# Performance work log

Hardware: AMD Instinct MI355X
Metric: run time of the kernel (lower is better)

The kernel has to match this reference:

```python
import math
import jax, jax.numpy as jnp
import numpy as np

B, S, D = 4, 2048, 1280
H, HD = 16, 80  # num_heads, head_dim
LOG2E = 1.442695041


def setup_inputs() -> dict:
    key = jax.random.key(0)
    ks = jax.random.split(key, 6)
    hidden_states = jax.random.normal(ks[0], (B, S, D), dtype=jnp.float32)
    # additive causal mask: 0 on/below diagonal, large negative above
    causal = jnp.tril(jnp.ones((S, S), dtype=bool))
    attention_mask = jnp.where(causal, 0.0, -1e9).astype(jnp.float32)[None, None, :, :]
    attention_mask = jnp.broadcast_to(attention_mask, (B, 1, S, S))
    scaling = jax.random.normal(ks[1], (HD,), dtype=jnp.float32)
    fan = 1.0 / math.sqrt(D)
    qkv_w = jax.random.normal(ks[2], (3 * H * HD, D), dtype=jnp.float32) * fan
    qkv_b = jax.random.normal(ks[3], (3 * H * HD,), dtype=jnp.float32) * fan
    o_w = jax.random.normal(ks[4], (D, H * HD), dtype=jnp.float32) * (1.0 / math.sqrt(H * HD))
    o_b = jax.random.normal(ks[5], (D,), dtype=jnp.float32) * fan
    return {
        "hidden_states": hidden_states,
        "attention_mask": attention_mask,
        "scaling": scaling,
        "qkv_w": qkv_w,
        "qkv_b": qkv_b,
        "o_w": o_w,
        "o_b": o_b,
    }


def reference(hidden_states, attention_mask, scaling, qkv_w, qkv_b, o_w, o_b):
    b, s, _ = hidden_states.shape
    qkv = hidden_states @ qkv_w.T + qkv_b  # [b, s, 3*H*HD]
    xq, xk, xv = jnp.split(qkv, [H * HD, 2 * H * HD], axis=-1)
    xq = xq.reshape(b, s, H, HD)
    xk = xk.reshape(b, s, H, HD)
    xv = xv.reshape(b, s, H, HD)
    # per-dim query scaling: softplus(scaling) * log2(e) / sqrt(head_dim)
    scale = jax.nn.softplus(scaling) * (LOG2E / math.sqrt(HD))
    xq = xq * scale[None, None, None, :]
    scores = jnp.einsum("bqhd,bkhd->bhqk", xq, xk) + attention_mask  # [b,H,s,s]
    probs = jax.nn.softmax(scores.astype(jnp.float32), axis=-1).astype(xq.dtype)
    out = jnp.einsum("bhqk,bkhd->bqhd", probs, xv).reshape(b, s, H * HD)
    return out @ o_w.T + o_b
```

## Files before the change

### kernel.cpp

```cpp
#include <hip/hip_runtime.h>
#include <math.h>

#define B_ 4
#define S_ 2048
#define D_ 1280
#define H_ 16
#define HD_ 80
#define HHD (H_ * HD_)
#define QKVN (3 * H_ * HD_)

typedef __bf16 bf16x8 __attribute__((ext_vector_type(8)));
typedef __bf16 bf16x4 __attribute__((ext_vector_type(4)));
typedef float  f32x4  __attribute__((ext_vector_type(4)));

__global__ __launch_bounds__(256) void cvt_bf16(
    const float* __restrict__ in, __bf16* __restrict__ out, int n8)
{
    const int i = blockIdx.x * 256 + threadIdx.x;
    if (i < n8) {
        const float4 a = ((const float4*)in)[2 * (size_t)i];
        const float4 b = ((const float4*)in)[2 * (size_t)i + 1];
        bf16x8 v = {(__bf16)a.x, (__bf16)a.y, (__bf16)a.z, (__bf16)a.w,
                    (__bf16)b.x, (__bf16)b.y, (__bf16)b.z, (__bf16)b.w};
        *(bf16x8*)(out + 8 * (size_t)i) = v;
    }
}

__device__ __forceinline__ void async_copy16(const void* g, void* l)
{
    __builtin_amdgcn_global_load_lds(
        (const __attribute__((address_space(1))) unsigned int*)g,
        (__attribute__((address_space(3))) unsigned int*)l, 16, 0, 0);
}

__device__ __forceinline__ void stage128x64(
    const __bf16* __restrict__ src, int K, char* lds, int tid)
{
    const int wave = tid >> 6, lane = tid & 63;
#pragma unroll
    for (int i = 0; i < 4; ++i) {
        const int c = (wave * 4 + i) * 64 + lane;
        const int r = c >> 3;
        const int g = (c & 7) ^ (r & 7);
        async_copy16(src + (size_t)r * K + g * 8, lds + (wave * 4 + i) * 1024);
    }
}

__device__ __forceinline__ bf16x8 frag_ld(const char* lds, int m, int j)
{
    return *(const bf16x8*)(lds + m * 128 + ((j ^ (m & 7)) << 4));
}

__device__ __forceinline__ void mfma_loop(
    const __bf16* __restrict__ A, const __bf16* __restrict__ W, int K,
    char* ldsA, char* ldsB, int tid, f32x4 acc[4][4])
{
    const int wave = tid >> 6;
    const int wm = wave >> 1, wn = wave & 1;
    const int l16 = tid & 15, quad = (tid & 63) >> 4;

#pragma unroll
    for (int mi = 0; mi < 4; ++mi)
#pragma unroll
        for (int ni = 0; ni < 4; ++ni) acc[mi][ni] = (f32x4){0.f, 0.f, 0.f, 0.f};

    for (int k0 = 0; k0 < K; k0 += 64) {
        __syncthreads();
        stage128x64(A + k0, K, ldsA, tid);
        stage128x64(W + k0, K, ldsB, tid);
        __syncthreads();
#pragma unroll
        for (int ks = 0; ks < 2; ++ks) {
            bf16x8 af[4], bfr[4];
#pragma unroll
            for (int mi = 0; mi < 4; ++mi)
                af[mi] = frag_ld(ldsA, wm * 64 + mi * 16 + l16, ks * 4 + quad);
#pragma unroll
            for (int ni = 0; ni < 4; ++ni)
                bfr[ni] = frag_ld(ldsB, wn * 64 + ni * 16 + l16, ks * 4 + quad);
#pragma unroll
            for (int mi = 0; mi < 4; ++mi)
#pragma unroll
                for (int ni = 0; ni < 4; ++ni)
                    acc[mi][ni] = __builtin_amdgcn_mfma_f32_16x16x32_bf16(
                        af[mi], bfr[ni], acc[mi][ni], 0, 0, 0);
        }
    }
}

__device__ __forceinline__ void stage_half256(
    const __bf16* __restrict__ src, int K, char* ldsmat, int half, int tid)
{
    const int wave = tid >> 6, lane = tid & 63;
#pragma unroll
    for (int i = 0; i < 2; ++i) {
        const int c = (i * 8 + wave) * 64 + lane;
        const int r = half * 128 + (c >> 3);
        const int g = (c & 7) ^ (r & 7);
        async_copy16(src + (size_t)r * K + g * 8,
                     ldsmat + half * 16384 + (i * 8 + wave) * 1024);
    }
}

#define QBAR() do { asm volatile("" ::: "memory");                             \
                    __builtin_amdgcn_s_barrier();                              \
                    __builtin_amdgcn_sched_barrier(0); } while (0)

__global__ __launch_bounds__(512, 2) void gemm_qkv_256(
    const __bf16* __restrict__ Ab, const __bf16* __restrict__ Wb,
    const float* __restrict__ bias, const float* __restrict__ scaling,
    __bf16* __restrict__ Qb, __bf16* __restrict__ Kb, __bf16* __restrict__ Vtb)
{
    __shared__ __align__(16) char lds[2][2][32768];
    const int tid = threadIdx.x;
    const int wave = tid >> 6;
    const int wm = wave >> 2, wn = wave & 3;
    const int l16 = tid & 15, quad = (tid & 63) >> 4;

    const int flat = blockIdx.x;
    const int xcd = flat & 7;
    const int idx = flat >> 3;
    const int m_i = idx & 3, n_g = idx >> 2;
    const int m0 = (xcd * 4 + m_i) * 256;
    const int n0 = n_g * 256;

    const __bf16* A = Ab + (size_t)m0 * D_;
    const __bf16* W = Wb + (size_t)n0 * D_;

    f32x4 acc[8][4];
#pragma unroll
    for (int mi = 0; mi < 8; ++mi)
#pragma unroll
        for (int ni = 0; ni < 4; ++ni) acc[mi][ni] = (f32x4){0.f, 0.f, 0.f, 0.f};

    stage_half256(A, D_, lds[0][0], 0, tid);
    stage_half256(A, D_, lds[0][0], 1, tid);
    stage_half256(W, D_, lds[0][1], 0, tid);
    stage_half256(W, D_, lds[0][1], 1, tid);

    const int nt = D_ / 64;
    bf16x8 af[4][2], bfr[2][2];

#define RD_A(MH)                                                               \
    _Pragma("unroll")                                                          \
    for (int mi = 0; mi < 4; ++mi)                                             \
        _Pragma("unroll")                                                      \
        for (int ks = 0; ks < 2; ++ks)                                         \
            af[mi][ks] = frag_ld(lA, wm * 128 + (MH) * 64 + mi * 16 + l16,     \
                                 ks * 4 + quad);
#define RD_B(NH)                                                               \
    _Pragma("unroll")                                                          \
    for (int ni = 0; ni < 2; ++ni)                                             \
        _Pragma("unroll")                                                      \
        for (int ks = 0; ks < 2; ++ks)                                         \
            bfr[ni][ks] = frag_ld(lB, wn * 64 + (NH) * 32 + ni * 16 + l16,     \
                                  ks * 4 + quad);
#define MM16(MH, NH)                                                           \
    __builtin_amdgcn_s_setprio(1);                                             \
    _Pragma("unroll")                                                          \
    for (int mi = 0; mi < 4; ++mi)                                             \
        _Pragma("unroll")                                                      \
        for (int ni = 0; ni < 2; ++ni) {                                       \
            acc[(MH)*4+mi][(NH)*2+ni] = __builtin_amdgcn_mfma_f32_16x16x32_bf16( \
                af[mi][0], bfr[ni][0], acc[(MH)*4+mi][(NH)*2+ni], 0, 0, 0);    \
            acc[(MH)*4+mi][(NH)*2+ni] = __builtin_amdgcn_mfma_f32_16x16x32_bf16( \
                af[mi][1], bfr[ni][1], acc[(MH)*4+mi][(NH)*2+ni], 0, 0, 0);    \
        }                                                                      \
    __builtin_amdgcn_s_setprio(0);

    for (int t = 0; t < nt; ++t) {
        const int cur = t & 1;
        const char* lA = lds[cur][0];
        const char* lB = lds[cur][1];
        char* sA = lds[cur ^ 1][0];
        char* sB = lds[cur ^ 1][1];
        const int kn = (t + 1 < nt ? t + 1 : t) * 64;

        stage_half256(A + kn, D_, sA, 0, tid);
        asm volatile("s_waitcnt vmcnt(2)" ::: "memory");
        QBAR();
        RD_A(0) RD_B(0) MM16(0, 0)
        stage_half256(A + kn, D_, sA, 1, tid);
        RD_B(1) MM16(0, 1)
        stage_half256(W + kn, D_, sB, 0, tid);
        RD_A(1) RD_B(0) MM16(1, 0)
        stage_half256(W + kn, D_, sB, 1, tid);
        RD_B(1) MM16(1, 1)
        QBAR();
    }
#undef RD_A
#undef RD_B
#undef MM16

    const int sec = n_g / 5;
    if (sec == 2) {
#pragma unroll
        for (int ni = 0; ni < 4; ++ni) {
            const int col = n0 + wn * 64 + ni * 16 + l16;
            const int cis = col - 2 * HHD;
            const int h = cis / HD_;
            const int d = cis - h * HD_;
            const float bv = bias[col];
#pragma unroll
            for (int mi = 0; mi < 8; ++mi) {
                const int row0 = m0 + wm * 128 + mi * 16 + quad * 4;
                const int bb = row0 >> 11;
                const int s = row0 & (S_ - 1);
                const size_t bh = (size_t)(bb * H_ + h);
                bf16x4 pv = {(__bf16)(acc[mi][ni][0] + bv),
                             (__bf16)(acc[mi][ni][1] + bv),
                             (__bf16)(acc[mi][ni][2] + bv),
                             (__bf16)(acc[mi][ni][3] + bv)};
                *(bf16x4*)(Vtb + (bh * HD_ + d) * S_ + s) = pv;
            }
        }
    } else {
#pragma unroll
        for (int ni = 0; ni < 4; ++ni) {
            const int col = n0 + wn * 64 + ni * 16 + l16;
            const int cis = col - sec * HHD;
            const int h = cis / HD_;
            const int d = cis - h * HD_;
            const float bv = bias[col];
            float qsv = 0.f;
            if (sec == 0)
                qsv = log1pf(expf(scaling[d])) *
                      (1.442695041f * 1.442695041f / 8.944271910f);
#pragma unroll
            for (int mi = 0; mi < 8; ++mi) {
#pragma unroll
                for (int r = 0; r < 4; ++r) {
                    const int row = m0 + wm * 128 + mi * 16 + quad * 4 + r;
                    const int bb = row >> 11;
                    const int s = row & (S_ - 1);
                    const size_t bh = (size_t)(bb * H_ + h);
                    const float v = acc[mi][ni][r] + bv;
                    if (sec == 0) Qb[(bh * S_ + s) * HD_ + d] = (__bf16)(v * qsv);
                    else          Kb[(bh * S_ + s) * HD_ + d] = (__bf16)v;
                }
            }
        }
    }
}

__global__ __launch_bounds__(256) void gemm_o_mfma(
    const __bf16* __restrict__ Ab, const __bf16* __restrict__ Wb,
    const float* __restrict__ bias, float* __restrict__ C)
{
    __shared__ __align__(16) char ldsA[128 * 128];
    __shared__ __align__(16) char ldsB[128 * 128];
    const int tid = threadIdx.x;

    const int flat = blockIdx.x;
    const int xcd = flat & 7;
    const int idx = flat >> 3;
    const int mm = idx / 10;
    const int nn = idx - mm * 10;
    const int m0 = (xcd * 8 + mm) * 128;
    const int n0 = nn * 128;

    f32x4 acc[4][4];
    mfma_loop(Ab + (size_t)m0 * D_, Wb + (size_t)n0 * D_, D_, ldsA, ldsB, tid, acc);

    const int wave = tid >> 6, wm = wave >> 1, wn = wave & 1;
    const int l16 = tid & 15, quad = (tid & 63) >> 4;

#pragma unroll
    for (int ni = 0; ni < 4; ++ni) {
        const int col = n0 + wn * 64 + ni * 16 + l16;
        const float bv = bias[col];
#pragma unroll
        for (int mi = 0; mi < 4; ++mi) {
#pragma unroll
            for (int r = 0; r < 4; ++r) {
                const int row = m0 + wm * 64 + mi * 16 + quad * 4 + r;
                C[(size_t)row * D_ + col] = acc[mi][ni][r] + bv;
            }
        }
    }
}

struct KF8 { bf16x8 f0, f1, f2; };

__device__ __forceinline__ void kload8(
    const __bf16* __restrict__ base, int row, int quad, KF8& kf)
{
    const __bf16* r = base + (size_t)row * HD_;
    kf.f0 = *(const bf16x8*)(r + quad * 8);
    kf.f1 = *(const bf16x8*)(r + 32 + quad * 8);
    bf16x8 z = {};
    if (quad < 2) z = *(const bf16x8*)(r + 64 + quad * 8);
    kf.f2 = z;
}

#define QK3(SREG, KF, QF)                                                      \
    SREG = __builtin_amdgcn_mfma_f32_16x16x32_bf16(KF.f0, QF.f0, SREG, 0, 0, 0); \
    SREG = __builtin_amdgcn_mfma_f32_16x16x32_bf16(KF.f1, QF.f1, SREG, 0, 0, 0); \
    SREG = __builtin_amdgcn_mfma_f32_16x16x32_bf16(KF.f2, QF.f2, SREG, 0, 0, 0);

#define MASK4(SREG, BASE, Q)                                                   \
    _Pragma("unroll")                                                          \
    for (int i = 0; i < 4; ++i)                                                \
        SREG[i] = ((BASE) + quad * 4 + i <= (Q) + l16) ? SREG[i] : -1e30f;

#define ATTN_BODY64(KT)                                                        \
    {                                                                          \
        const int k0 = (KT) * 64;                                              \
        const bool do_lo = ((KT) < nkt_lo);                  \
        const bf16x8 vf00 = *(const bf16x8*)(Vbase + (size_t)( 0 + l16) * S_ + k0 + quad * 8);      \
        const bf16x8 vf01 = *(const bf16x8*)(Vbase + (size_t)( 0 + l16) * S_ + k0 + 32 + quad * 8); \
        const bf16x8 vf10 = *(const bf16x8*)(Vbase + (size_t)(16 + l16) * S_ + k0 + quad * 8);      \
        const bf16x8 vf11 = *(const bf16x8*)(Vbase + (size_t)(16 + l16) * S_ + k0 + 32 + quad * 8); \
        const bf16x8 vf20 = *(const bf16x8*)(Vbase + (size_t)(32 + l16) * S_ + k0 + quad * 8);      \
        const bf16x8 vf21 = *(const bf16x8*)(Vbase + (size_t)(32 + l16) * S_ + k0 + 32 + quad * 8); \
        const bf16x8 vf30 = *(const bf16x8*)(Vbase + (size_t)(48 + l16) * S_ + k0 + quad * 8);      \
        const bf16x8 vf31 = *(const bf16x8*)(Vbase + (size_t)(48 + l16) * S_ + k0 + 32 + quad * 8); \
        const bf16x8 vf40 = *(const bf16x8*)(Vbase + (size_t)(64 + l16) * S_ + k0 + quad * 8);      \
        const bf16x8 vf41 = *(const bf16x8*)(Vbase + (size_t)(64 + l16) * S_ + k0 + 32 + quad * 8); \
        f32x4 sH0 = (f32x4){0.f,0.f,0.f,0.f}, sH1 = sH0, sH2 = sH0, sH3 = sH0; \
        f32x4 sL0 = sH0, sL1 = sH0, sL2 = sH0, sL3 = sH0;                      \
        __builtin_amdgcn_s_setprio(1);                                         \
        QK3(sH0, kf0, qfH) QK3(sH1, kf1, qfH) QK3(sH2, kf2, qfH) QK3(sH3, kf3, qfH) \
        if (do_lo) {                                                           \
            QK3(sL0, kf0, qfL) QK3(sL1, kf1, qfL)                              \
            QK3(sL2, kf2, qfL) QK3(sL3, kf3, qfL)                              \
        }                                                                      \
        __builtin_amdgcn_s_setprio(0);                                         \
        {                                                                      \
            const int kn = ((KT) + 1 < nkt_hi ? (KT) + 1 : (KT)) * 64;         \
            kload8(Kbase, kn + l16, quad, kf0);                                \
            kload8(Kbase, kn + 16 + l16, quad, kf1);                           \
            kload8(Kbase, kn + 32 + l16, quad, kf2);                           \
            kload8(Kbase, kn + 48 + l16, quad, kf3);                           \
        }                                                                      \
        float aH;                                                              \
        {                                                                      \
            if (k0 + 63 > q_hi) {                                              \
                MASK4(sH0, k0, q_hi)      MASK4(sH1, k0 + 16, q_hi)            \
                MASK4(sH2, k0 + 32, q_hi) MASK4(sH3, k0 + 48, q_hi)            \
            }                                                                  \
            float mA = fmaxf(fmaxf(sH0[0], sH0[1]), fmaxf(sH0[2], sH0[3]));    \
            float mB = fmaxf(fmaxf(sH1[0], sH1[1]), fmaxf(sH1[2], sH1[3]));    \
            float mC = fmaxf(fmaxf(sH2[0], sH2[1]), fmaxf(sH2[2], sH2[3]));    \
            float mD = fmaxf(fmaxf(sH3[0], sH3[1]), fmaxf(sH3[2], sH3[3]));    \
            float mx = fmaxf(fmaxf(mA, mB), fmaxf(mC, mD));                    \
            mx = fmaxf(mx, __shfl_xor(mx, 16));                                \
            mx = fmaxf(mx, __shfl_xor(mx, 32));                                \
            const float mn = fmaxf(mH, mx);                                    \
            aH = exp2f(mH - mn);                                               \
            mH = mn;                                                           \
            float rs = 0.f;                                                    \
            _Pragma("unroll")                                                  \
            for (int i = 0; i < 4; ++i) {                                      \
                const float p0 = exp2f(sH0[i] - mn);                           \
                const float p1 = exp2f(sH1[i] - mn);                           \
                const float p2 = exp2f(sH2[i] - mn);                           \
                const float p3 = exp2f(sH3[i] - mn);                           \
                sH0[i] = p0; sH1[i] = p1; sH2[i] = p2; sH3[i] = p3;            \
                rs += (p0 + p1) + (p2 + p3);                                   \
            }                                                                  \
            lH = lH * aH + rs;                                                 \
            *(bf16x4*)&Ps[wave][0][l16][0][quad * 4] =                         \
                (bf16x4){(__bf16)sH0[0], (__bf16)sH0[1], (__bf16)sH0[2], (__bf16)sH0[3]}; \
            *(bf16x4*)&Ps[wave][0][l16][0][16 + quad * 4] =                    \
                (bf16x4){(__bf16)sH1[0], (__bf16)sH1[1], (__bf16)sH1[2], (__bf16)sH1[3]}; \
            *(bf16x4*)&Ps[wave][0][l16][1][quad * 4] =                         \
                (bf16x4){(__bf16)sH2[0], (__bf16)sH2[1], (__bf16)sH2[2], (__bf16)sH2[3]}; \
            *(bf16x4*)&Ps[wave][0][l16][1][16 + quad * 4] =                    \
                (bf16x4){(__bf16)sH3[0], (__bf16)sH3[1], (__bf16)sH3[2], (__bf16)sH3[3]}; \
        }                                                                      \
        float aL = 1.f;                                                        \
        if (do_lo) {                                                           \
            if (k0 + 63 > q_lo) {                                              \
                MASK4(sL0, k0, q_lo)      MASK4(sL1, k0 + 16, q_lo)            \
                MASK4(sL2, k0 + 32, q_lo) MASK4(sL3, k0 + 48, q_lo)            \
            }                                                                  \
            float mA = fmaxf(fmaxf(sL0[0], sL0[1]), fmaxf(sL0[2], sL0[3]));    \
            float mB = fmaxf(fmaxf(sL1[0], sL1[1]), fmaxf(sL1[2], sL1[3]));    \
            float mC = fmaxf(fmaxf(sL2[0], sL2[1]), fmaxf(sL2[2], sL2[3]));    \
            float mD = fmaxf(fmaxf(sL3[0], sL3[1]), fmaxf(sL3[2], sL3[3]));    \
            float mx = fmaxf(fmaxf(mA, mB), fmaxf(mC, mD));                    \
            mx = fmaxf(mx, __shfl_xor(mx, 16));                                \
            mx = fmaxf(mx, __shfl_xor(mx, 32));                                \
            const float mn = fmaxf(mL, mx);                                    \
            aL = exp2f(mL - mn);                                               \
            mL = mn;                                                           \
            float rs = 0.f;                                                    \
            _Pragma("unroll")                                                  \
            for (int i = 0; i < 4; ++i) {                                      \
                const float p0 = exp2f(sL0[i] - mn);                           \
                const float p1 = exp2f(sL1[i] - mn);                           \
                const float p2 = exp2f(sL2[i] - mn);                           \
                const float p3 = exp2f(sL3[i] - mn);                           \
                sL0[i] = p0; sL1[i] = p1; sL2[i] = p2; sL3[i] = p3;            \
                rs += (p0 + p1) + (p2 + p3);                                   \
            }                                                                  \
            lL = lL * aL + rs;                                                 \
            *(bf16x4*)&Ps[wave][1][l16][0][quad * 4] =                         \
                (bf16x4){(__bf16)sL0[0], (__bf16)sL0[1], (__bf16)sL0[2], (__bf16)sL0[3]}; \
            *(bf16x4*)&Ps[wave][1][l16][0][16 + quad * 4] =                    \
                (bf16x4){(__bf16)sL1[0], (__bf16)sL1[1], (__bf16)sL1[2], (__bf16)sL1[3]}; \
            *(bf16x4*)&Ps[wave][1][l16][1][quad * 4] =                         \
                (bf16x4){(__bf16)sL2[0], (__bf16)sL2[1], (__bf16)sL2[2], (__bf16)sL2[3]}; \
            *(bf16x4*)&Ps[wave][1][l16][1][16 + quad * 4] =                    \
                (bf16x4){(__bf16)sL3[0], (__bf16)sL3[1], (__bf16)sL3[2], (__bf16)sL3[3]}; \
        }                                                                      \
        asm volatile("s_waitcnt lgkmcnt(0)" ::: "memory");                     \
        const bf16x8 pfH0 = *(const bf16x8*)&Ps[wave][0][l16][0][quad * 8];    \
        const bf16x8 pfH1 = *(const bf16x8*)&Ps[wave][0][l16][1][quad * 8];    \
        const bf16x8 pfL0 = *(const bf16x8*)&Ps[wave][1][l16][0][quad * 8];    \
        const bf16x8 pfL1 = *(const bf16x8*)&Ps[wave][1][l16][1][quad * 8];    \
        __builtin_amdgcn_s_setprio(1);                                         \
        {                                                                      \
            f32x4 c0, c1, c2, c3, c4;                                          \
            _Pragma("unroll")                                                  \
            for (int i = 0; i < 4; ++i) {                                      \
                c0[i] = oH0[i] * aH; c1[i] = oH1[i] * aH; c2[i] = oH2[i] * aH; \
                c3[i] = oH3[i] * aH; c4[i] = oH4[i] * aH;                      \
            }                                                                  \
            oH0 = __builtin_amdgcn_mfma_f32_16x16x32_bf16(vf00, pfH0, c0, 0, 0, 0); \
            oH1 = __builtin_amdgcn_mfma_f32_16x16x32_bf16(vf10, pfH0, c1, 0, 0, 0); \
            oH2 = __builtin_amdgcn_mfma_f32_16x16x32_bf16(vf20, pfH0, c2, 0, 0, 0); \
            oH3 = __builtin_amdgcn_mfma_f32_16x16x32_bf16(vf30, pfH0, c3, 0, 0, 0); \
            oH4 = __builtin_amdgcn_mfma_f32_16x16x32_bf16(vf40, pfH0, c4, 0, 0, 0); \
            oH0 = __builtin_amdgcn_mfma_f32_16x16x32_bf16(vf01, pfH1, oH0, 0, 0, 0); \
            oH1 = __builtin_amdgcn_mfma_f32_16x16x32_bf16(vf11, pfH1, oH1, 0, 0, 0); \
            oH2 = __builtin_amdgcn_mfma_f32_16x16x32_bf16(vf21, pfH1, oH2, 0, 0, 0); \
            oH3 = __builtin_amdgcn_mfma_f32_16x16x32_bf16(vf31, pfH1, oH3, 0, 0, 0); \
            oH4 = __builtin_amdgcn_mfma_f32_16x16x32_bf16(vf41, pfH1, oH4, 0, 0, 0); \
        }                                                                      \
        if (do_lo) {                                                           \
            f32x4 c0, c1, c2, c3, c4;                                          \
            _Pragma("unroll")                                                  \
            for (int i = 0; i < 4; ++i) {                                      \
                c0[i] = oL0[i] * aL; c1[i] = oL1[i] * aL; c2[i] = oL2[i] * aL; \
                c3[i] = oL3[i] * aL; c4[i] = oL4[i] * aL;                      \
            }                                                                  \
            oL0 = __builtin_amdgcn_mfma_f32_16x16x32_bf16(vf00, pfL0, c0, 0, 0, 0); \
            oL1 = __builtin_amdgcn_mfma_f32_16x16x32_bf16(vf10, pfL0, c1, 0, 0, 0); \
            oL2 = __builtin_amdgcn_mfma_f32_16x16x32_bf16(vf20, pfL0, c2, 0, 0, 0); \
            oL3 = __builtin_amdgcn_mfma_f32_16x16x32_bf16(vf30, pfL0, c3, 0, 0, 0); \
            oL4 = __builtin_amdgcn_mfma_f32_16x16x32_bf16(vf40, pfL0, c4, 0, 0, 0); \
            oL0 = __builtin_amdgcn_mfma_f32_16x16x32_bf16(vf01, pfL1, oL0, 0, 0, 0); \
            oL1 = __builtin_amdgcn_mfma_f32_16x16x32_bf16(vf11, pfL1, oL1, 0, 0, 0); \
            oL2 = __builtin_amdgcn_mfma_f32_16x16x32_bf16(vf21, pfL1, oL2, 0, 0, 0); \
            oL3 = __builtin_amdgcn_mfma_f32_16x16x32_bf16(vf31, pfL1, oL3, 0, 0, 0); \
            oL4 = __builtin_amdgcn_mfma_f32_16x16x32_bf16(vf41, pfL1, oL4, 0, 0, 0); \
        }                                                                      \
        __builtin_amdgcn_s_setprio(0);                                         \
    }

__global__ __launch_bounds__(256, 2) void attn_v13(
    const __bf16* __restrict__ Qb, const __bf16* __restrict__ Kb,
    const __bf16* __restrict__ Vtb, __bf16* __restrict__ out)
{
    __shared__ __align__(16) __bf16 Ps[4][2][16][2][40];

    const int tid = threadIdx.x;
    const int wave = tid >> 6;
    const int lane = tid & 63;
    const int l16 = lane & 15;
    const int quad = lane >> 4;

    const int flat = blockIdx.x;
    const int c = flat & 7;
    const int slot = flat >> 3;
    const int bhgrp = slot >> 4;
    const int xslot = slot & 15;
    const int bh = bhgrp * 8 + c;
    const int x = (xslot + 5 * bhgrp) & 15;
    const int b = bh >> 4, h = bh & 15;

    const int q_lo = 64 * x + 16 * wave;
    const int q_hi = 64 * (31 - x) + 16 * wave;

    const __bf16* Qbase = Qb + (size_t)bh * S_ * HD_;
    const __bf16* Kbase = Kb + (size_t)bh * S_ * HD_;
    const __bf16* Vbase = Vtb + (size_t)bh * HD_ * S_;

    KF8 qfL, qfH;
    kload8(Qbase, q_lo + l16, quad, qfL);
    kload8(Qbase, q_hi + l16, quad, qfH);

    float mL = -1e30f, lL = 0.f, mH = -1e30f, lH = 0.f;
    f32x4 oH0 = (f32x4){0.f,0.f,0.f,0.f}, oH1 = oH0, oH2 = oH0, oH3 = oH0, oH4 = oH0;
    f32x4 oL0 = oH0, oL1 = oH0, oL2 = oH0, oL3 = oH0, oL4 = oH0;

    const int nkt_lo = (q_lo + 16 + 63) >> 6;
    const int nkt_hi = (q_hi + 16 + 63) >> 6;

    KF8 kf0, kf1, kf2, kf3;
    kload8(Kbase, l16, quad, kf0);
    kload8(Kbase, 16 + l16, quad, kf1);
    kload8(Kbase, 32 + l16, quad, kf2);
    kload8(Kbase, 48 + l16, quad, kf3);

    for (int kt = 0; kt < nkt_hi; ++kt) {
        ATTN_BODY64(kt);
    }

    float lHs = lH + __shfl_xor(lH, 16);
    lHs += __shfl_xor(lHs, 32);
    float lLs = lL + __shfl_xor(lL, 16);
    lLs += __shfl_xor(lLs, 32);
    const float invH = 1.f / lHs;
    const float invL = 1.f / lLs;
    const size_t rowH = ((size_t)b * S_ + q_hi + l16) * HHD + h * HD_ + quad * 4;
    const size_t rowL = ((size_t)b * S_ + q_lo + l16) * HHD + h * HD_ + quad * 4;
    {
        bf16x4 v0 = {(__bf16)(oH0[0]*invH), (__bf16)(oH0[1]*invH), (__bf16)(oH0[2]*invH), (__bf16)(oH0[3]*invH)};
        bf16x4 v1 = {(__bf16)(oH1[0]*invH), (__bf16)(oH1[1]*invH), (__bf16)(oH1[2]*invH), (__bf16)(oH1[3]*invH)};
        bf16x4 v2 = {(__bf16)(oH2[0]*invH), (__bf16)(oH2[1]*invH), (__bf16)(oH2[2]*invH), (__bf16)(oH2[3]*invH)};
        bf16x4 v3 = {(__bf16)(oH3[0]*invH), (__bf16)(oH3[1]*invH), (__bf16)(oH3[2]*invH), (__bf16)(oH3[3]*invH)};
        bf16x4 v4 = {(__bf16)(oH4[0]*invH), (__bf16)(oH4[1]*invH), (__bf16)(oH4[2]*invH), (__bf16)(oH4[3]*invH)};
        *(bf16x4*)(out + rowH)      = v0;
        *(bf16x4*)(out + rowH + 16) = v1;
        *(bf16x4*)(out + rowH + 32) = v2;
        *(bf16x4*)(out + rowH + 48) = v3;
        *(bf16x4*)(out + rowH + 64) = v4;
    }
    {
        bf16x4 v0 = {(__bf16)(oL0[0]*invL), (__bf16)(oL0[1]*invL), (__bf16)(oL0[2]*invL), (__bf16)(oL0[3]*invL)};
        bf16x4 v1 = {(__bf16)(oL1[0]*invL), (__bf16)(oL1[1]*invL), (__bf16)(oL1[2]*invL), (__bf16)(oL1[3]*invL)};
        bf16x4 v2 = {(__bf16)(oL2[0]*invL), (__bf16)(oL2[1]*invL), (__bf16)(oL2[2]*invL), (__bf16)(oL2[3]*invL)};
        bf16x4 v3 = {(__bf16)(oL3[0]*invL), (__bf16)(oL3[1]*invL), (__bf16)(oL3[2]*invL), (__bf16)(oL3[3]*invL)};
        bf16x4 v4 = {(__bf16)(oL4[0]*invL), (__bf16)(oL4[1]*invL), (__bf16)(oL4[2]*invL), (__bf16)(oL4[3]*invL)};
        *(bf16x4*)(out + rowL)      = v0;
        *(bf16x4*)(out + rowL + 16) = v1;
        *(bf16x4*)(out + rowL + 32) = v2;
        *(bf16x4*)(out + rowL + 48) = v3;
        *(bf16x4*)(out + rowL + 64) = v4;
    }
}

extern "C" void kernel_launch(void* const* d_in, const int* in_sizes, int n_in,
                              void* d_out, int out_size, void* d_ws, size_t ws_size,
                              hipStream_t stream)
{
    const float* hidden  = (const float*)d_in[0];
    const float* scaling = (const float*)d_in[2];
    const float* qkv_w   = (const float*)d_in[3];
    const float* qkv_b   = (const float*)d_in[4];
    const float* o_w     = (const float*)d_in[5];
    const float* o_b     = (const float*)d_in[6];
    float* out = (float*)d_out;

    const size_t N_HID = (size_t)B_ * S_ * D_;
    const size_t N_QW  = (size_t)QKVN * D_;
    const size_t N_OW  = (size_t)D_ * D_;
    const size_t NPH   = (size_t)B_ * H_ * S_ * HD_;

    __bf16* Ab    = (__bf16*)d_ws;
    __bf16* Wqb   = Ab + N_HID;
    __bf16* Wob   = Wqb + N_QW;
    __bf16* Qb    = Wob + N_OW;
    __bf16* Kb    = Qb + NPH;
    __bf16* Vtb   = Kb + NPH;
    __bf16* attnb = Vtb + NPH;

    dim3 blk(256);

    cvt_bf16<<<dim3(N_HID / 8 / 256), blk, 0, stream>>>(hidden, Ab, N_HID / 8);
    cvt_bf16<<<dim3(N_QW  / 8 / 256), blk, 0, stream>>>(qkv_w, Wqb, N_QW / 8);
    cvt_bf16<<<dim3(N_OW  / 8 / 256), blk, 0, stream>>>(o_w,   Wob, N_OW / 8);

    gemm_qkv_256<<<dim3(480), dim3(512), 0, stream>>>(
        Ab, Wqb, qkv_b, scaling, Qb, Kb, Vtb);

    attn_v13<<<dim3(16 * H_ * B_), blk, 0, stream>>>(Qb, Kb, Vtb, attnb);

    gemm_o_mfma<<<dim3(D_ / 128 * (B_ * S_ / 128)), blk, 0, stream>>>(
        attnb, Wob, o_b, out);
}
```

Measured before the change: 463.2 us.

## Merge bf16 conversions into one launch and use pipelined 256-tile O-projection GEMM

The three fp32-to-bf16 conversion launches become one kernel that picks its source buffer from the global thread index, removing two launches. The output-projection GEMM moves from a 128x128 tile with a synchronous single-buffered K loop to the double-buffered 256x256 pipeline already used by the QKV GEMM, now shared through a macro. Larger tiles raise data reuse and overlap loads with MFMA work. The cost is that the O GEMM launches only 160 workgroups, which may under-fill the GPU's compute units.

Measured after the change: 445.5 us. -3.8%, faster.

```diff
diff --git a/kernel.cpp b/kernel.cpp
--- a/kernel.cpp
+++ b/kernel.cpp
@@ -13,17 +13,27 @@
 typedef __bf16 bf16x4 __attribute__((ext_vector_type(4)));
 typedef float  f32x4  __attribute__((ext_vector_type(4)));
 
-__global__ __launch_bounds__(256) void cvt_bf16(
-    const float* __restrict__ in, __bf16* __restrict__ out, int n8)
-{
-    const int i = blockIdx.x * 256 + threadIdx.x;
-    if (i < n8) {
-        const float4 a = ((const float4*)in)[2 * (size_t)i];
-        const float4 b = ((const float4*)in)[2 * (size_t)i + 1];
-        bf16x8 v = {(__bf16)a.x, (__bf16)a.y, (__bf16)a.z, (__bf16)a.w,
-                    (__bf16)b.x, (__bf16)b.y, (__bf16)b.z, (__bf16)b.w};
-        *(bf16x8*)(out + 8 * (size_t)i) = v;
-    }
+__global__ __launch_bounds__(256) void cvt_all(
+    const float* __restrict__ h,  __bf16* __restrict__ hb,
+    const float* __restrict__ qw, __bf16* __restrict__ qwb,
+    const float* __restrict__ ow, __bf16* __restrict__ owb)
+{
+    const int n0 = (B_ * S_ * D_) / 8;
+    const int n1 = (QKVN * D_) / 8;
+    const int g = blockIdx.x * 256 + threadIdx.x;
+
+    const float* in;
+    __bf16* out;
+    int i;
+    if (g < n0)            { in = h;  out = hb;  i = g; }
+    else if (g < n0 + n1)  { in = qw; out = qwb; i = g - n0; }
+    else                   { in = ow; out = owb; i = g - n0 - n1; }
+
+    const float4 a = ((const float4*)in)[2 * (size_t)i];
+    const float4 b = ((const float4*)in)[2 * (size_t)i + 1];
+    bf16x8 v = {(__bf16)a.x, (__bf16)a.y, (__bf16)a.z, (__bf16)a.w,
+                (__bf16)b.x, (__bf16)b.y, (__bf16)b.z, (__bf16)b.w};
+    *(bf16x8*)(out + 8 * (size_t)i) = v;
 }
 
 __device__ __forceinline__ void async_copy16(const void* g, void* l)
@@ -33,59 +43,9 @@
         (__attribute__((address_space(3))) unsigned int*)l, 16, 0, 0);
 }
 
-__device__ __forceinline__ void stage128x64(
-    const __bf16* __restrict__ src, int K, char* lds, int tid)
-{
-    const int wave = tid >> 6, lane = tid & 63;
-#pragma unroll
-    for (int i = 0; i < 4; ++i) {
-        const int c = (wave * 4 + i) * 64 + lane;
-        const int r = c >> 3;
-        const int g = (c & 7) ^ (r & 7);
-        async_copy16(src + (size_t)r * K + g * 8, lds + (wave * 4 + i) * 1024);
-    }
-}
-
 __device__ __forceinline__ bf16x8 frag_ld(const char* lds, int m, int j)
 {
     return *(const bf16x8*)(lds + m * 128 + ((j ^ (m & 7)) << 4));
-}
-
-__device__ __forceinline__ void mfma_loop(
-    const __bf16* __restrict__ A, const __bf16* __restrict__ W, int K,
-    char* ldsA, char* ldsB, int tid, f32x4 acc[4][4])
-{
-    const int wave = tid >> 6;
-    const int wm = wave >> 1, wn = wave & 1;
-    const int l16 = tid & 15, quad = (tid & 63) >> 4;
-
-#pragma unroll
-    for (int mi = 0; mi < 4; ++mi)
-#pragma unroll
-        for (int ni = 0; ni < 4; ++ni) acc[mi][ni] = (f32x4){0.f, 0.f, 0.f, 0.f};
-
-    for (int k0 = 0; k0 < K; k0 += 64) {
-        __syncthreads();
-        stage128x64(A + k0, K, ldsA, tid);
-        stage128x64(W + k0, K, ldsB, tid);
-        __syncthreads();
-#pragma unroll
-        for (int ks = 0; ks < 2; ++ks) {
-            bf16x8 af[4], bfr[4];
-#pragma unroll
-            for (int mi = 0; mi < 4; ++mi)
-                af[mi] = frag_ld(ldsA, wm * 64 + mi * 16 + l16, ks * 4 + quad);
-#pragma unroll
-            for (int ni = 0; ni < 4; ++ni)
-                bfr[ni] = frag_ld(ldsB, wn * 64 + ni * 16 + l16, ks * 4 + quad);
-#pragma unroll
-            for (int mi = 0; mi < 4; ++mi)
-#pragma unroll
-                for (int ni = 0; ni < 4; ++ni)
-                    acc[mi][ni] = __builtin_amdgcn_mfma_f32_16x16x32_bf16(
-                        af[mi], bfr[ni], acc[mi][ni], 0, 0, 0);
-        }
-    }
 }
 
 __device__ __forceinline__ void stage_half256(
@@ -105,41 +65,6 @@
 #define QBAR() do { asm volatile("" ::: "memory");                             \
                     __builtin_amdgcn_s_barrier();                              \
                     __builtin_amdgcn_sched_barrier(0); } while (0)
-
-__global__ __launch_bounds__(512, 2) void gemm_qkv_256(
-    const __bf16* __restrict__ Ab, const __bf16* __restrict__ Wb,
-    const float* __restrict__ bias, const float* __restrict__ scaling,
-    __bf16* __restrict__ Qb, __bf16* __restrict__ Kb, __bf16* __restrict__ Vtb)
-{
-    __shared__ __align__(16) char lds[2][2][32768];
-    const int tid = threadIdx.x;
-    const int wave = tid >> 6;
-    const int wm = wave >> 2, wn = wave & 3;
-    const int l16 = tid & 15, quad = (tid & 63) >> 4;
-
-    const int flat = blockIdx.x;
-    const int xcd = flat & 7;
-    const int idx = flat >> 3;
-    const int m_i = idx & 3, n_g = idx >> 2;
-    const int m0 = (xcd * 4 + m_i) * 256;
-    const int n0 = n_g * 256;
-
-    const __bf16* A = Ab + (size_t)m0 * D_;
-    const __bf16* W = Wb + (size_t)n0 * D_;
-
-    f32x4 acc[8][4];
-#pragma unroll
-    for (int mi = 0; mi < 8; ++mi)
-#pragma unroll
-        for (int ni = 0; ni < 4; ++ni) acc[mi][ni] = (f32x4){0.f, 0.f, 0.f, 0.f};
-
-    stage_half256(A, D_, lds[0][0], 0, tid);
-    stage_half256(A, D_, lds[0][0], 1, tid);
-    stage_half256(W, D_, lds[0][1], 0, tid);
-    stage_half256(W, D_, lds[0][1], 1, tid);
-
-    const int nt = D_ / 64;
-    bf16x8 af[4][2], bfr[2][2];
 
 #define RD_A(MH)                                                               \
     _Pragma("unroll")                                                          \
@@ -168,29 +93,63 @@
         }                                                                      \
     __builtin_amdgcn_s_setprio(0);
 
-    for (int t = 0; t < nt; ++t) {
-        const int cur = t & 1;
-        const char* lA = lds[cur][0];
-        const char* lB = lds[cur][1];
-        char* sA = lds[cur ^ 1][0];
-        char* sB = lds[cur ^ 1][1];
-        const int kn = (t + 1 < nt ? t + 1 : t) * 64;
-
-        stage_half256(A + kn, D_, sA, 0, tid);
-        asm volatile("s_waitcnt vmcnt(2)" ::: "memory");
-        QBAR();
-        RD_A(0) RD_B(0) MM16(0, 0)
-        stage_half256(A + kn, D_, sA, 1, tid);
-        RD_B(1) MM16(0, 1)
-        stage_half256(W + kn, D_, sB, 0, tid);
-        RD_A(1) RD_B(0) MM16(1, 0)
-        stage_half256(W + kn, D_, sB, 1, tid);
-        RD_B(1) MM16(1, 1)
-        QBAR();
-    }
-#undef RD_A
-#undef RD_B
-#undef MM16
+#define GEMM256_PIPELINE(A_, W_)                                               \
+    stage_half256(A_, D_, lds[0][0], 0, tid);                                  \
+    stage_half256(A_, D_, lds[0][0], 1, tid);                                  \
+    stage_half256(W_, D_, lds[0][1], 0, tid);                                  \
+    stage_half256(W_, D_, lds[0][1], 1, tid);                                  \
+    for (int t = 0; t < nt; ++t) {                                             \
+        const int cur = t & 1;                                                 \
+        const char* lA = lds[cur][0];                                          \
+        const char* lB = lds[cur][1];                                          \
+        char* sA = lds[cur ^ 1][0];                                            \
+        char* sB = lds[cur ^ 1][1];                                            \
+        const int kn = (t + 1 < nt ? t + 1 : t) * 64;                          \
+                     \
+        stage_half256(A_ + kn, D_, sA, 0, tid);                                \
+        asm volatile("s_waitcnt vmcnt(2)" ::: "memory");                       \
+        QBAR();                                                                \
+        RD_A(0) RD_B(0) MM16(0, 0)                                             \
+        stage_half256(A_ + kn, D_, sA, 1, tid);                                \
+        RD_B(1) MM16(0, 1)                                                     \
+        stage_half256(W_ + kn, D_, sB, 0, tid);                                \
+        RD_A(1) RD_B(0) MM16(1, 0)                                             \
+        stage_half256(W_ + kn, D_, sB, 1, tid);                                \
+        RD_B(1) MM16(1, 1)                                                     \
+        QBAR();                                                                \
+    }
+
+__global__ __launch_bounds__(512, 2) void gemm_qkv_256(
+    const __bf16* __restrict__ Ab, const __bf16* __restrict__ Wb,
+    const float* __restrict__ bias, const float* __restrict__ scaling,
+    __bf16* __restrict__ Qb, __bf16* __restrict__ Kb, __bf16* __restrict__ Vtb)
+{
+    __shared__ __align__(16) char lds[2][2][32768];
+    const int tid = threadIdx.x;
+    const int wave = tid >> 6;
+    const int wm = wave >> 2, wn = wave & 3;
+    const int l16 = tid & 15, quad = (tid & 63) >> 4;
+
+    const int flat = blockIdx.x;
+    const int xcd = flat & 7;
+    const int idx = flat >> 3;
+    const int m_i = idx & 3, n_g = idx >> 2;
+    const int m0 = (xcd * 4 + m_i) * 256;
+    const int n0 = n_g * 256;
+
+    const __bf16* A = Ab + (size_t)m0 * D_;
+    const __bf16* W = Wb + (size_t)n0 * D_;
+
+    f32x4 acc[8][4];
+#pragma unroll
+    for (int mi = 0; mi < 8; ++mi)
+#pragma unroll
+        for (int ni = 0; ni < 4; ++ni) acc[mi][ni] = (f32x4){0.f, 0.f, 0.f, 0.f};
+
+    const int nt = D_ / 64;
+    bf16x8 af[4][2], bfr[2][2];
+
+    GEMM256_PIPELINE(A, W)
 
     const int sec = n_g / 5;
     if (sec == 2) {
@@ -243,37 +202,46 @@
     }
 }
 
-__global__ __launch_bounds__(256) void gemm_o_mfma(
+__global__ __launch_bounds__(512, 2) void gemm_o_256(
     const __bf16* __restrict__ Ab, const __bf16* __restrict__ Wb,
     const float* __restrict__ bias, float* __restrict__ C)
 {
-    __shared__ __align__(16) char ldsA[128 * 128];
-    __shared__ __align__(16) char ldsB[128 * 128];
+    __shared__ __align__(16) char lds[2][2][32768];
     const int tid = threadIdx.x;
+    const int wave = tid >> 6;
+    const int wm = wave >> 2, wn = wave & 3;
+    const int l16 = tid & 15, quad = (tid & 63) >> 4;
 
     const int flat = blockIdx.x;
     const int xcd = flat & 7;
     const int idx = flat >> 3;
-    const int mm = idx / 10;
-    const int nn = idx - mm * 10;
-    const int m0 = (xcd * 8 + mm) * 128;
-    const int n0 = nn * 128;
-
-    f32x4 acc[4][4];
-    mfma_loop(Ab + (size_t)m0 * D_, Wb + (size_t)n0 * D_, D_, ldsA, ldsB, tid, acc);
-
-    const int wave = tid >> 6, wm = wave >> 1, wn = wave & 1;
-    const int l16 = tid & 15, quad = (tid & 63) >> 4;
+    const int m_i = idx & 3, n_g = idx >> 2;
+    const int m0 = (xcd * 4 + m_i) * 256;
+    const int n0 = n_g * 256;
+
+    const __bf16* A = Ab + (size_t)m0 * D_;
+    const __bf16* W = Wb + (size_t)n0 * D_;
+
+    f32x4 acc[8][4];
+#pragma unroll
+    for (int mi = 0; mi < 8; ++mi)
+#pragma unroll
+        for (int ni = 0; ni < 4; ++ni) acc[mi][ni] = (f32x4){0.f, 0.f, 0.f, 0.f};
+
+    const int nt = D_ / 64;
+    bf16x8 af[4][2], bfr[2][2];
+
+    GEMM256_PIPELINE(A, W)
 
 #pragma unroll
     for (int ni = 0; ni < 4; ++ni) {
         const int col = n0 + wn * 64 + ni * 16 + l16;
         const float bv = bias[col];
 #pragma unroll
-        for (int mi = 0; mi < 4; ++mi) {
+        for (int mi = 0; mi < 8; ++mi) {
 #pragma unroll
             for (int r = 0; r < 4; ++r) {
-                const int row = m0 + wm * 64 + mi * 16 + quad * 4 + r;
+                const int row = m0 + wm * 128 + mi * 16 + quad * 4 + r;
                 C[(size_t)row * D_ + col] = acc[mi][ni][r] + bv;
             }
         }
@@ -558,17 +526,16 @@
     __bf16* Vtb   = Kb + NPH;
     __bf16* attnb = Vtb + NPH;
 
-    dim3 blk(256);
-
-    cvt_bf16<<<dim3(N_HID / 8 / 256), blk, 0, stream>>>(hidden, Ab, N_HID / 8);
-    cvt_bf16<<<dim3(N_QW  / 8 / 256), blk, 0, stream>>>(qkv_w, Wqb, N_QW / 8);
-    cvt_bf16<<<dim3(N_OW  / 8 / 256), blk, 0, stream>>>(o_w,   Wob, N_OW / 8);
+    const int cvt_blocks = (int)((N_HID + N_QW + N_OW) / 8 / 256);
+
+    cvt_all<<<dim3(cvt_blocks), dim3(256), 0, stream>>>(
+        hidden, Ab, qkv_w, Wqb, o_w, Wob);
 
     gemm_qkv_256<<<dim3(480), dim3(512), 0, stream>>>(
         Ab, Wqb, qkv_b, scaling, Qb, Kb, Vtb);
 
-    attn_v13<<<dim3(16 * H_ * B_), blk, 0, stream>>>(Qb, Kb, Vtb, attnb);
-
-    gemm_o_mfma<<<dim3(D_ / 128 * (B_ * S_ / 128)), blk, 0, stream>>>(
+    attn_v13<<<dim3(16 * H_ * B_), dim3(256), 0, stream>>>(Qb, Kb, Vtb, attnb);
+
+    gemm_o_256<<<dim3(160), dim3(512), 0, stream>>>(
         attnb, Wob, o_b, out);
 }
```
